# Kernel optimization log

Hardware: AMD Instinct MI355X
Metric: run time of the kernel (lower is better)

## Reference

```python
import jax, jax.numpy as jnp
import numpy as np

N_NODES = 50000
N_EDGES = 800000
D = 128
N_LAYERS = 4
NUM_GRAPHS = 128
BN_EPS = 1e-5


def setup_inputs() -> dict:
    key = jax.random.key(0)
    ks = jax.random.split(key, 10)
    x = jax.random.normal(ks[0], (N_NODES, D), dtype=jnp.float32)
    edge_index = jax.random.randint(ks[1], (2, N_EDGES), 0, N_NODES, dtype=jnp.int64)
    batch = jnp.sort(jax.random.randint(ks[2], (N_NODES,), 0, NUM_GRAPHS, dtype=jnp.int64))
    # GINConv MLP params: Linear(D->D), ReLU, Linear(D->D); stacked over layers.
    scale = 1.0 / np.sqrt(D)
    W1 = jax.random.normal(ks[3], (N_LAYERS, D, D), dtype=jnp.float32) * scale
    b1 = jnp.zeros((N_LAYERS, D), dtype=jnp.float32)
    W2 = jax.random.normal(ks[4], (N_LAYERS, D, D), dtype=jnp.float32) * scale
    b2 = jnp.zeros((N_LAYERS, D), dtype=jnp.float32)
    eps = jnp.zeros((N_LAYERS,), dtype=jnp.float32)  # train_eps=True, init 0
    bn_gamma = jnp.ones((N_LAYERS - 1, D), dtype=jnp.float32)
    bn_beta = jnp.zeros((N_LAYERS - 1, D), dtype=jnp.float32)
    return {"x": x, "edge_index": edge_index, "batch": batch,
            "W1": W1, "b1": b1, "W2": W2, "b2": b2, "eps": eps,
            "bn_gamma": bn_gamma, "bn_beta": bn_beta}


def reference(x, edge_index, batch, W1, b1, W2, b2, eps, bn_gamma, bn_beta):
    src, dst = edge_index[0], edge_index[1]
    h = x
    for i in range(N_LAYERS):
        # GINConv: MLP((1+eps)*x_i + sum_{j->i} x_j)
        agg = jax.ops.segment_sum(h[src], dst, num_segments=N_NODES)  # [N, D]
        z = (1.0 + eps[i]) * h + agg
        z = jnp.maximum(z @ W1[i] + b1[i], 0.0) @ W2[i] + b2[i]
        if i < N_LAYERS - 1:
            # BatchNorm1d (training-mode batch statistics) + ReLU
            mu = jnp.mean(z, axis=0)
            var = jnp.var(z, axis=0)
            z = (z - mu) * jax.lax.rsqrt(var + BN_EPS) * bn_gamma[i] + bn_beta[i]
            z = jnp.maximum(z, 0.0)
        h = z
    # global_add_pool
    return jax.ops.segment_sum(h, batch, num_segments=NUM_GRAPHS)  # [G, D]
```

## Files before the change

kernel.cpp:

```cpp
#include <hip/hip_runtime.h>

#define N_NODES 50000
#define N_EDGES 800000
#define D 128
#define NUM_GRAPHS 128

typedef __attribute__((ext_vector_type(8)))  short bfrag8;
typedef __attribute__((ext_vector_type(16))) float f32x16;

__device__ __forceinline__ float4 f4zero() { return make_float4(0.f, 0.f, 0.f, 0.f); }

__device__ __forceinline__ unsigned short f2bf(float f) {
    unsigned u = __float_as_uint(f);
    unsigned r = (u + 0x7fffu + ((u >> 16) & 1u)) >> 16;
    return (unsigned short)r;
}
__device__ __forceinline__ float bf2f(unsigned short b) {
    return __uint_as_float(((unsigned)b) << 16);
}
__device__ __forceinline__ float4 bf2f4(ushort4 u) {
    return make_float4(bf2f(u.x), bf2f(u.y), bf2f(u.z), bf2f(u.w));
}
__device__ __forceinline__ void acc4(float4& a, float4 u) {
    a.x += u.x; a.y += u.y; a.z += u.z; a.w += u.w;
}
__device__ __forceinline__ void acc8(float* a, uint4 r) {
    a[0] += __uint_as_float(r.x << 16);
    a[1] += __uint_as_float(r.x & 0xffff0000u);
    a[2] += __uint_as_float(r.y << 16);
    a[3] += __uint_as_float(r.y & 0xffff0000u);
    a[4] += __uint_as_float(r.z << 16);
    a[5] += __uint_as_float(r.z & 0xffff0000u);
    a[6] += __uint_as_float(r.w << 16);
    a[7] += __uint_as_float(r.w & 0xffff0000u);
}

__global__ __launch_bounds__(256) void prep_kernel(
    const float* __restrict__ W1, const float* __restrict__ W2,
    const float* __restrict__ x, short* __restrict__ Wt,
    ushort4* __restrict__ Hb, int* __restrict__ deg, float* __restrict__ stats)
{
    int b = blockIdx.x, t = threadIdx.x;
    if (b < 512) {
        int idx = b * 256 + t;
        int m = idx >> 14, rem = idx & 16383;
        int k = rem >> 7, n = rem & 127;
        const float* W = (m < 4) ? (W1 + (size_t)m * 16384)
                                 : (W2 + (size_t)(m - 4) * 16384);
        Wt[(size_t)m * 16384 + n * 128 + k] = (short)f2bf(W[k * 128 + n]);
    } else if (b < 6762) {
        int i = (b - 512) * 256 + t;
        float4 v = ((const float4*)x)[i];
        Hb[i] = make_ushort4(f2bf(v.x), f2bf(v.y), f2bf(v.z), f2bf(v.w));
    } else if (b < 6958) {
        int i = (b - 6762) * 256 + t;
        if (i < N_NODES) deg[i] = 0;
    } else {
        int i = (b - 6958) * 256 + t;
        stats[i] = 0.f;
    }
}

__global__ __launch_bounds__(256) void hist_kernel(
    const int* __restrict__ dst, int* __restrict__ deg,
    int* __restrict__ edge_pos)
{
    int e = blockIdx.x * 256 + threadIdx.x;
    if (e < N_EDGES) edge_pos[e] = atomicAdd(&deg[dst[e]], 1);
}

__global__ __launch_bounds__(256) void scan_block_kernel(
    const int* __restrict__ deg, int* __restrict__ row_ptr,
    int* __restrict__ blockSum)
{
    __shared__ int wsum[4];
    int t = threadIdx.x, b = blockIdx.x;
    int i = b * 256 + t;
    int v = (i < N_NODES) ? deg[i] : 0;
    int lane = t & 63, wid = t >> 6;
    #pragma unroll
    for (int off = 1; off < 64; off <<= 1) {
        int u = __shfl_up(v, off, 64);
        if (lane >= off) v += u;
    }
    if (lane == 63) wsum[wid] = v;
    __syncthreads();
    int add = 0;
    for (int w = 0; w < wid; ++w) add += wsum[w];
    v += add;
    if (i < N_NODES) row_ptr[i + 1] = v;
    if (t == 255) blockSum[b] = v;
}

__global__ __launch_bounds__(256) void scan_fixup_kernel(
    const int* __restrict__ blockSum, int* __restrict__ row_ptr, int nb)
{
    __shared__ int wsum[4];
    __shared__ int sbuf[256];
    int t = threadIdx.x, b = blockIdx.x;
    int v = (t < nb) ? blockSum[t] : 0;
    int lane = t & 63, wid = t >> 6;
    #pragma unroll
    for (int off = 1; off < 64; off <<= 1) {
        int u = __shfl_up(v, off, 64);
        if (lane >= off) v += u;
    }
    if (lane == 63) wsum[wid] = v;
    __syncthreads();
    int add = 0;
    for (int w = 0; w < wid; ++w) add += wsum[w];
    sbuf[t] = v + add;
    __syncthreads();
    if (b == 0 && t == 0) row_ptr[0] = 0;
    if (b > 0) {
        int off = sbuf[b - 1];
        int i = b * 256 + t;
        if (i < N_NODES) row_ptr[i + 1] += off;
    }
}

__global__ __launch_bounds__(256) void fill_kernel(
    const int* __restrict__ src, const int* __restrict__ dst,
    const int* __restrict__ row_ptr, const int* __restrict__ edge_pos,
    int* __restrict__ csr_src)
{
    int e = blockIdx.x * 256 + threadIdx.x;
    if (e >= N_EDGES) return;
    csr_src[row_ptr[dst[e]] + edge_pos[e]] = src[e];
}

__global__ __launch_bounds__(256) void bnapply_kernel(
    uint4* __restrict__ H, const float* __restrict__ stats,
    const float* __restrict__ gamma, const float* __restrict__ beta)
{
    __shared__ float sa[128], sb[128];
    int tid = threadIdx.x;
    if (tid < 128) {
        const float invN = 1.0f / (float)N_NODES;
        float m = stats[tid] * invN;
        float a = gamma[tid] * rsqrtf(stats[128 + tid] * invN - m * m + 1e-5f);
        sa[tid] = a;
        sb[tid] = beta[tid] - m * a;
    }
    __syncthreads();
    int id = blockIdx.x * 256 + tid;
    int c0 = (id & 15) * 8;
    uint4 u = H[id];
    float lo, hi;
    lo = fmaxf(sa[c0 + 0] * __uint_as_float(u.x << 16)          + sb[c0 + 0], 0.f);
    hi = fmaxf(sa[c0 + 1] * __uint_as_float(u.x & 0xffff0000u) + sb[c0 + 1], 0.f);
    u.x = (unsigned)f2bf(lo) | ((unsigned)f2bf(hi) << 16);
    lo = fmaxf(sa[c0 + 2] * __uint_as_float(u.y << 16)          + sb[c0 + 2], 0.f);
    hi = fmaxf(sa[c0 + 3] * __uint_as_float(u.y & 0xffff0000u) + sb[c0 + 3], 0.f);
    u.y = (unsigned)f2bf(lo) | ((unsigned)f2bf(hi) << 16);
    lo = fmaxf(sa[c0 + 4] * __uint_as_float(u.z << 16)          + sb[c0 + 4], 0.f);
    hi = fmaxf(sa[c0 + 5] * __uint_as_float(u.z & 0xffff0000u) + sb[c0 + 5], 0.f);
    u.z = (unsigned)f2bf(lo) | ((unsigned)f2bf(hi) << 16);
    lo = fmaxf(sa[c0 + 6] * __uint_as_float(u.w << 16)          + sb[c0 + 6], 0.f);
    hi = fmaxf(sa[c0 + 7] * __uint_as_float(u.w & 0xffff0000u) + sb[c0 + 7], 0.f);
    u.w = (unsigned)f2bf(lo) | ((unsigned)f2bf(hi) << 16);
    H[id] = u;
}

__global__ __launch_bounds__(256) void gather_kernel(
    const uint4* __restrict__ H, const int* __restrict__ row_ptr,
    const int* __restrict__ csr_src, const float* __restrict__ epsp,
    uint4* __restrict__ A)
{
    int node = blockIdx.x * 16 + (threadIdx.x >> 4);
    int lane = threadIdx.x & 15;
    float eps1 = 1.0f + *epsp;
    int beg = row_ptr[node], end = row_ptr[node + 1];

    uint4 hv = H[node * 16 + lane];
    float acc[8];
    acc[0] = eps1 * __uint_as_float(hv.x << 16);
    acc[1] = eps1 * __uint_as_float(hv.x & 0xffff0000u);
    acc[2] = eps1 * __uint_as_float(hv.y << 16);
    acc[3] = eps1 * __uint_as_float(hv.y & 0xffff0000u);
    acc[4] = eps1 * __uint_as_float(hv.z << 16);
    acc[5] = eps1 * __uint_as_float(hv.z & 0xffff0000u);
    acc[6] = eps1 * __uint_as_float(hv.w << 16);
    acc[7] = eps1 * __uint_as_float(hv.w & 0xffff0000u);

    for (int base = beg; base < end; base += 16) {
        int idx = (base + lane < end) ? csr_src[base + lane] : 0;
        int cnt = min(16, end - base);
        int j = 0;
        for (; j + 8 <= cnt; j += 8) {
            int s0 = __shfl(idx, j + 0, 16), s1 = __shfl(idx, j + 1, 16);
            int s2 = __shfl(idx, j + 2, 16), s3 = __shfl(idx, j + 3, 16);
            int s4 = __shfl(idx, j + 4, 16), s5 = __shfl(idx, j + 5, 16);
            int s6 = __shfl(idx, j + 6, 16), s7 = __shfl(idx, j + 7, 16);
            uint4 u0 = H[s0 * 16 + lane];
            uint4 u1 = H[s1 * 16 + lane];
            uint4 u2 = H[s2 * 16 + lane];
            uint4 u3 = H[s3 * 16 + lane];
            uint4 u4 = H[s4 * 16 + lane];
            uint4 u5 = H[s5 * 16 + lane];
            uint4 u6 = H[s6 * 16 + lane];
            uint4 u7 = H[s7 * 16 + lane];
            acc8(acc, u0); acc8(acc, u1); acc8(acc, u2); acc8(acc, u3);
            acc8(acc, u4); acc8(acc, u5); acc8(acc, u6); acc8(acc, u7);
        }
        for (; j + 4 <= cnt; j += 4) {
            int s0 = __shfl(idx, j + 0, 16), s1 = __shfl(idx, j + 1, 16);
            int s2 = __shfl(idx, j + 2, 16), s3 = __shfl(idx, j + 3, 16);
            uint4 u0 = H[s0 * 16 + lane];
            uint4 u1 = H[s1 * 16 + lane];
            uint4 u2 = H[s2 * 16 + lane];
            uint4 u3 = H[s3 * 16 + lane];
            acc8(acc, u0); acc8(acc, u1); acc8(acc, u2); acc8(acc, u3);
        }
        for (; j < cnt; ++j) {
            int s = __shfl(idx, j, 16);
            uint4 u = H[s * 16 + lane];
            acc8(acc, u);
        }
    }
    uint4 o;
    o.x = (unsigned)f2bf(acc[0]) | ((unsigned)f2bf(acc[1]) << 16);
    o.y = (unsigned)f2bf(acc[2]) | ((unsigned)f2bf(acc[3]) << 16);
    o.z = (unsigned)f2bf(acc[4]) | ((unsigned)f2bf(acc[5]) << 16);
    o.w = (unsigned)f2bf(acc[6]) | ((unsigned)f2bf(acc[7]) << 16);
    A[node * 16 + lane] = o;
}

__global__ __launch_bounds__(256, 3) void mlp_fused_kernel(
    const ushort* __restrict__ A,
    const short* __restrict__ Wt1,
    const short* __restrict__ Wt2,
    const float* __restrict__ bias1,
    const float* __restrict__ bias2,
    ushort* __restrict__ Hout,
    float* __restrict__ statsSum,
    float* __restrict__ statsSq,
    int M)
{
    __shared__ __align__(16) short Wlds[128 * 128];
    __shared__ __align__(16) short zlds[2][32 * 128];
    __shared__ float ssum[128];
    __shared__ float ssq[128];

    const int tid  = threadIdx.x;
    const int wv   = tid >> 6;
    const int lane = tid & 63;
    const int half = lane >> 5;
    const int ln   = lane & 31;
    const int rg   = wv & 1;
    const int ch   = wv >> 1;
    const int row0 = blockIdx.x * 64 + rg * 32;
    const bool doStats = (statsSum != nullptr);
    if (doStats && tid < 128) { ssum[tid] = 0.f; ssq[tid] = 0.f; }

    short* zw = &zlds[rg][0];

    {
        const int4* Wg = (const int4*)Wt1;
        int4* Wl = (int4*)Wlds;
        #pragma unroll
        for (int i = 0; i < 8; ++i) {
            int id = i * 256 + tid;
            int n = id >> 4, c = id & 15;
            Wl[n * 16 + (c ^ (n & 15))] = Wg[id];
        }
    }
    __syncthreads();

    {
        f32x16 acc[2];
        #pragma unroll
        for (int ci = 0; ci < 2; ++ci)
            #pragma unroll
            for (int r = 0; r < 16; ++r) acc[ci][r] = 0.f;

        bfrag8 af[8];
        int rowc = min(row0 + ln, M - 1);
        const ushort* ap = A + (size_t)rowc * 128 + half * 8;
        #pragma unroll
        for (int kk = 0; kk < 8; ++kk)
            af[kk] = *(const bfrag8*)(ap + kk * 16);

        #pragma unroll
        for (int kk = 0; kk < 8; ++kk) {
            #pragma unroll
            for (int ci = 0; ci < 2; ++ci) {
                int n = (ch * 2 + ci) * 32 + ln;
                int c = kk * 2 + half;
                bfrag8 bf = *(const bfrag8*)(Wlds + n * 128 + ((c ^ (n & 15)) << 3));
                acc[ci] = __builtin_amdgcn_mfma_f32_32x32x16_bf16(
                    af[kk], bf, acc[ci], 0, 0, 0);
            }
        }
        #pragma unroll
        for (int ci = 0; ci < 2; ++ci) {
            int col = (ch * 2 + ci) * 32 + ln;
            int cc = col >> 3, co = col & 7;
            float bv = bias1[col];
            #pragma unroll
            for (int r = 0; r < 16; ++r) {
                int rloc = (r & 3) + 8 * (r >> 2) + 4 * half;
                float v = fmaxf(acc[ci][r] + bv, 0.f);
                zw[rloc * 128 + ((cc ^ (rloc & 15)) << 3) + co] = (short)f2bf(v);
            }
        }
    }
    __syncthreads();

    bfrag8 af2[8];
    #pragma unroll
    for (int kk = 0; kk < 8; ++kk) {
        int c = kk * 2 + half;
        af2[kk] = *(const bfrag8*)(zw + ln * 128 + ((c ^ (ln & 15)) << 3));
    }
    {
        const int4* Wg = (const int4*)Wt2;
        int4* Wl = (int4*)Wlds;
        #pragma unroll
        for (int i = 0; i < 8; ++i) {
            int id = i * 256 + tid;
            int n = id >> 4, c = id & 15;
            Wl[n * 16 + (c ^ (n & 15))] = Wg[id];
        }
    }
    __syncthreads();

    {
        f32x16 acc[2];
        #pragma unroll
        for (int ci = 0; ci < 2; ++ci)
            #pragma unroll
            for (int r = 0; r < 16; ++r) acc[ci][r] = 0.f;

        #pragma unroll
        for (int kk = 0; kk < 8; ++kk) {
            #pragma unroll
            for (int ci = 0; ci < 2; ++ci) {
                int n = (ch * 2 + ci) * 32 + ln;
                int c = kk * 2 + half;
                bfrag8 bf = *(const bfrag8*)(Wlds + n * 128 + ((c ^ (n & 15)) << 3));
                acc[ci] = __builtin_amdgcn_mfma_f32_32x32x16_bf16(
                    af2[kk], bf, acc[ci], 0, 0, 0);
            }
        }
        #pragma unroll
        for (int ci = 0; ci < 2; ++ci) {
            int col = (ch * 2 + ci) * 32 + ln;
            int cc = col >> 3, co = col & 7;
            float bv = bias2[col];
            float s = 0.f, sq = 0.f;
            #pragma unroll
            for (int r = 0; r < 16; ++r) {
                int rloc = (r & 3) + 8 * (r >> 2) + 4 * half;
                float v = acc[ci][r] + bv;
                zw[rloc * 128 + ((cc ^ (rloc & 15)) << 3) + co] = (short)f2bf(v);
                if (row0 + rloc < M) { s += v; sq += v * v; }
            }
            if (doStats) {
                s  += __shfl_xor(s, 32);
                sq += __shfl_xor(sq, 32);
                if (half == 0) {
                    atomicAdd(&ssum[col], s);
                    atomicAdd(&ssq[col], sq);
                }
            }
        }
    }
    __syncthreads();

    {
        int4* Ho = (int4*)Hout;
        #pragma unroll
        for (int i = 0; i < 4; ++i) {
            int id = i * 256 + tid;
            int r = id >> 4, c = id & 15;
            int rl = r & 31;
            int grow = blockIdx.x * 64 + r;
            if (grow < M)
                Ho[(size_t)grow * 16 + c] =
                    ((const int4*)&zlds[r >> 5][0])[rl * 16 + (c ^ (rl & 15))];
        }
    }
    if (doStats && tid < 128) {
        atomicAdd(&statsSum[tid], ssum[tid]);
        atomicAdd(&statsSq[tid],  ssq[tid]);
    }
}

__global__ __launch_bounds__(256) void pool_kernel(
    const ushort4* __restrict__ H, const int* __restrict__ batch,
    float* __restrict__ out)
{
    int c4 = threadIdx.x & 31;
    int nl = threadIdx.x >> 5;
    int node0 = blockIdx.x * 256;
    float4 acc = f4zero();
    int gcur = -1;
    for (int i = nl; i < 256; i += 8) {
        int n = node0 + i;
        if (n >= N_NODES) break;
        int g = batch[n];
        if (g != gcur) {
            if (gcur >= 0) {
                float* o = out + gcur * D + c4 * 4;
                atomicAdd(o + 0, acc.x); atomicAdd(o + 1, acc.y);
                atomicAdd(o + 2, acc.z); atomicAdd(o + 3, acc.w);
            }
            gcur = g;
            acc = f4zero();
        }
        float4 v = bf2f4(H[n * 32 + c4]);
        acc4(acc, v);
    }
    if (gcur >= 0) {
        float* o = out + gcur * D + c4 * 4;
        atomicAdd(o + 0, acc.x); atomicAdd(o + 1, acc.y);
        atomicAdd(o + 2, acc.z); atomicAdd(o + 3, acc.w);
    }
}

extern "C" void kernel_launch(void* const* d_in, const int* in_sizes, int n_in,
                              void* d_out, int out_size, void* d_ws, size_t ws_size,
                              hipStream_t stream)
{
    const float* x     = (const float*)d_in[0];
    const int*   ei    = (const int*)d_in[1];
    const int*   batch = (const int*)d_in[2];
    const float* W1    = (const float*)d_in[3];
    const float* b1    = (const float*)d_in[4];
    const float* W2    = (const float*)d_in[5];
    const float* b2    = (const float*)d_in[6];
    const float* eps   = (const float*)d_in[7];
    const float* gamma = (const float*)d_in[8];
    const float* beta  = (const float*)d_in[9];
    float* out = (float*)d_out;

    unsigned short* Hb  = (unsigned short*)d_ws;
    unsigned short* Abf = Hb + (size_t)N_NODES * D;
    float* stats    = (float*)(Abf + (size_t)N_NODES * D);
    int*   deg      = (int*)(stats + 3 * 256);
    int*   row_ptr  = deg + N_NODES;
    int*   blockSum = row_ptr + N_NODES + 1;
    int*   edge_pos = blockSum + 256;
    int*   csr_src  = edge_pos + N_EDGES;
    short* Wt       = (short*)(csr_src + N_EDGES);

    const int* src = ei;
    const int* dst = ei + N_EDGES;

    const int edgeBlocks   = (N_EDGES + 255) / 256;
    const int scanBlocks   = (N_NODES + 255) / 256;
    const int gatherBlocks = (N_NODES + 15) / 16;
    const int bnBlocks     = (N_NODES * 16) / 256;
    const int gemmBlocks   = (N_NODES + 63) / 64;

    prep_kernel<<<6961, 256, 0, stream>>>(W1, W2, x, Wt, (ushort4*)Hb,
                                          deg, stats);
    hist_kernel<<<edgeBlocks, 256, 0, stream>>>(dst, deg, edge_pos);
    scan_block_kernel<<<scanBlocks, 256, 0, stream>>>(deg, row_ptr, blockSum);
    scan_fixup_kernel<<<scanBlocks, 256, 0, stream>>>(blockSum, row_ptr, scanBlocks);
    fill_kernel<<<edgeBlocks, 256, 0, stream>>>(src, dst, row_ptr, edge_pos, csr_src);

    for (int layer = 0; layer < 4; ++layer) {
        const bool bn = (layer < 3);
        if (layer > 0) {
            bnapply_kernel<<<bnBlocks, 256, 0, stream>>>(
                (uint4*)Hb, stats + (size_t)(layer - 1) * 256,
                gamma + (size_t)(layer - 1) * D, beta + (size_t)(layer - 1) * D);
        }
        gather_kernel<<<gatherBlocks, 256, 0, stream>>>(
            (const uint4*)Hb, row_ptr, csr_src, eps + layer, (uint4*)Abf);
        mlp_fused_kernel<<<gemmBlocks, 256, 0, stream>>>(
            Abf, Wt + (size_t)layer * 16384, Wt + (size_t)(4 + layer) * 16384,
            b1 + (size_t)layer * D, b2 + (size_t)layer * D, Hb,
            bn ? stats + layer * 256 : nullptr,
            bn ? stats + layer * 256 + 128 : nullptr, N_NODES);
    }

    hipMemsetAsync(out, 0, (size_t)NUM_GRAPHS * D * sizeof(float), stream);
    pool_kernel<<<scanBlocks, 256, 0, stream>>>(
        (const ushort4*)Hb, batch, out);
}
```

Measured before the change: 411.6 us.

## Pad CSR rows to multiples of eight, use 16-bit indices, fuse pooling into MLP

CSR rows are padded to a multiple of 8 and the padding slots point at an extra zeroed dummy node, so the gather loop runs branch-light 8- or 16-wide batches with no remainder loops. It also prefetches the next index chunk. Edge positions and source indices are stored as 16-bit values to halve index traffic, and gather gets an occupancy hint. The final global add-pool is fused into the last MLP kernel's epilogue, which removes the separate pool kernel and the write and reread of the last layer's H. The cost is extra padded entries in the gather and an implicit limit that node IDs and per-node degrees fit in 16 bits.

```diff
diff --git a/kernel.cpp b/kernel.cpp
--- a/kernel.cpp
+++ b/kernel.cpp
@@ -17,12 +17,6 @@
 }
 __device__ __forceinline__ float bf2f(unsigned short b) {
     return __uint_as_float(((unsigned)b) << 16);
-}
-__device__ __forceinline__ float4 bf2f4(ushort4 u) {
-    return make_float4(bf2f(u.x), bf2f(u.y), bf2f(u.z), bf2f(u.w));
-}
-__device__ __forceinline__ void acc4(float4& a, float4 u) {
-    a.x += u.x; a.y += u.y; a.z += u.z; a.w += u.w;
 }
 __device__ __forceinline__ void acc8(float* a, uint4 r) {
     a[0] += __uint_as_float(r.x << 16);
@@ -55,18 +49,20 @@
     } else if (b < 6958) {
         int i = (b - 6762) * 256 + t;
         if (i < N_NODES) deg[i] = 0;
-    } else {
+    } else if (b < 6961) {
         int i = (b - 6958) * 256 + t;
         stats[i] = 0.f;
+    } else {
+        if (t < 64) ((unsigned*)Hb)[(size_t)N_NODES * 64 + t] = 0u;
     }
 }
 
 __global__ __launch_bounds__(256) void hist_kernel(
     const int* __restrict__ dst, int* __restrict__ deg,
-    int* __restrict__ edge_pos)
+    unsigned short* __restrict__ edge_pos)
 {
     int e = blockIdx.x * 256 + threadIdx.x;
-    if (e < N_EDGES) edge_pos[e] = atomicAdd(&deg[dst[e]], 1);
+    if (e < N_EDGES) edge_pos[e] = (unsigned short)atomicAdd(&deg[dst[e]], 1);
 }
 
 __global__ __launch_bounds__(256) void scan_block_kernel(
@@ -76,7 +72,7 @@
     __shared__ int wsum[4];
     int t = threadIdx.x, b = blockIdx.x;
     int i = b * 256 + t;
-    int v = (i < N_NODES) ? deg[i] : 0;
+    int v = (i < N_NODES) ? ((deg[i] + 7) & ~7) : 0;
     int lane = t & 63, wid = t >> 6;
     #pragma unroll
     for (int off = 1; off < 64; off <<= 1) {
@@ -121,12 +117,23 @@
 
 __global__ __launch_bounds__(256) void fill_kernel(
     const int* __restrict__ src, const int* __restrict__ dst,
-    const int* __restrict__ row_ptr, const int* __restrict__ edge_pos,
-    int* __restrict__ csr_src)
-{
-    int e = blockIdx.x * 256 + threadIdx.x;
-    if (e >= N_EDGES) return;
-    csr_src[row_ptr[dst[e]] + edge_pos[e]] = src[e];
+    const int* __restrict__ row_ptr, const unsigned short* __restrict__ edge_pos,
+    const int* __restrict__ deg, unsigned short* __restrict__ csr_src)
+{
+    int b = blockIdx.x, t = threadIdx.x;
+    if (b < 3125) {
+        int e = b * 256 + t;
+        if (e < N_EDGES)
+            csr_src[row_ptr[dst[e]] + (int)edge_pos[e]] = (unsigned short)src[e];
+    } else {
+        int n = (b - 3125) * 256 + t;
+        if (n < N_NODES) {
+            int e0 = row_ptr[n] + deg[n];
+            int e1 = row_ptr[n + 1];
+            for (int j = e0; j < e1; ++j)
+                csr_src[j] = (unsigned short)N_NODES;
+        }
+    }
 }
 
 __global__ __launch_bounds__(256) void bnapply_kernel(
@@ -162,9 +169,9 @@
     H[id] = u;
 }
 
-__global__ __launch_bounds__(256) void gather_kernel(
+__global__ __launch_bounds__(256, 4) void gather_kernel(
     const uint4* __restrict__ H, const int* __restrict__ row_ptr,
-    const int* __restrict__ csr_src, const float* __restrict__ epsp,
+    const unsigned short* __restrict__ csr, const float* __restrict__ epsp,
     uint4* __restrict__ A)
 {
     int node = blockIdx.x * 16 + (threadIdx.x >> 4);
@@ -172,7 +179,7 @@
     float eps1 = 1.0f + *epsp;
     int beg = row_ptr[node], end = row_ptr[node + 1];
 
-    uint4 hv = H[node * 16 + lane];
+    uint4 hv = H[(size_t)node * 16 + lane];
     float acc[8];
     acc[0] = eps1 * __uint_as_float(hv.x << 16);
     acc[1] = eps1 * __uint_as_float(hv.x & 0xffff0000u);
@@ -183,47 +190,54 @@
     acc[6] = eps1 * __uint_as_float(hv.w << 16);
     acc[7] = eps1 * __uint_as_float(hv.w & 0xffff0000u);
 
-    for (int base = beg; base < end; base += 16) {
-        int idx = (base + lane < end) ? csr_src[base + lane] : 0;
-        int cnt = min(16, end - base);
-        int j = 0;
-        for (; j + 8 <= cnt; j += 8) {
-            int s0 = __shfl(idx, j + 0, 16), s1 = __shfl(idx, j + 1, 16);
-            int s2 = __shfl(idx, j + 2, 16), s3 = __shfl(idx, j + 3, 16);
-            int s4 = __shfl(idx, j + 4, 16), s5 = __shfl(idx, j + 5, 16);
-            int s6 = __shfl(idx, j + 6, 16), s7 = __shfl(idx, j + 7, 16);
-            uint4 u0 = H[s0 * 16 + lane];
-            uint4 u1 = H[s1 * 16 + lane];
-            uint4 u2 = H[s2 * 16 + lane];
-            uint4 u3 = H[s3 * 16 + lane];
-            uint4 u4 = H[s4 * 16 + lane];
-            uint4 u5 = H[s5 * 16 + lane];
-            uint4 u6 = H[s6 * 16 + lane];
-            uint4 u7 = H[s7 * 16 + lane];
+    int base = beg;
+    int idx = (int)csr[base + lane];
+    while (base < end) {
+        int nb = base + 16;
+        int nidx = 0;
+        if (nb < end) nidx = (int)csr[nb + lane];
+        int cnt = end - base;
+        int s0 = __shfl(idx, 0, 16), s1 = __shfl(idx, 1, 16);
+        int s2 = __shfl(idx, 2, 16), s3 = __shfl(idx, 3, 16);
+        int s4 = __shfl(idx, 4, 16), s5 = __shfl(idx, 5, 16);
+        int s6 = __shfl(idx, 6, 16), s7 = __shfl(idx, 7, 16);
+        uint4 u0 = H[(size_t)s0 * 16 + lane];
+        uint4 u1 = H[(size_t)s1 * 16 + lane];
+        uint4 u2 = H[(size_t)s2 * 16 + lane];
+        uint4 u3 = H[(size_t)s3 * 16 + lane];
+        uint4 u4 = H[(size_t)s4 * 16 + lane];
+        uint4 u5 = H[(size_t)s5 * 16 + lane];
+        uint4 u6 = H[(size_t)s6 * 16 + lane];
+        uint4 u7 = H[(size_t)s7 * 16 + lane];
+        if (cnt > 8) {
+            int t0 = __shfl(idx,  8, 16), t1 = __shfl(idx,  9, 16);
+            int t2 = __shfl(idx, 10, 16), t3 = __shfl(idx, 11, 16);
+            int t4 = __shfl(idx, 12, 16), t5 = __shfl(idx, 13, 16);
+            int t6 = __shfl(idx, 14, 16), t7 = __shfl(idx, 15, 16);
+            uint4 w0 = H[(size_t)t0 * 16 + lane];
+            uint4 w1 = H[(size_t)t1 * 16 + lane];
+            uint4 w2 = H[(size_t)t2 * 16 + lane];
+            uint4 w3 = H[(size_t)t3 * 16 + lane];
+            uint4 w4 = H[(size_t)t4 * 16 + lane];
+            uint4 w5 = H[(size_t)t5 * 16 + lane];
+            uint4 w6 = H[(size_t)t6 * 16 + lane];
+            uint4 w7 = H[(size_t)t7 * 16 + lane];
             acc8(acc, u0); acc8(acc, u1); acc8(acc, u2); acc8(acc, u3);
             acc8(acc, u4); acc8(acc, u5); acc8(acc, u6); acc8(acc, u7);
-        }
-        for (; j + 4 <= cnt; j += 4) {
-            int s0 = __shfl(idx, j + 0, 16), s1 = __shfl(idx, j + 1, 16);
-            int s2 = __shfl(idx, j + 2, 16), s3 = __shfl(idx, j + 3, 16);
-            uint4 u0 = H[s0 * 16 + lane];
-            uint4 u1 = H[s1 * 16 + lane];
-            uint4 u2 = H[s2 * 16 + lane];
-            uint4 u3 = H[s3 * 16 + lane];
+            acc8(acc, w0); acc8(acc, w1); acc8(acc, w2); acc8(acc, w3);
+            acc8(acc, w4); acc8(acc, w5); acc8(acc, w6); acc8(acc, w7);
+        } else {
             acc8(acc, u0); acc8(acc, u1); acc8(acc, u2); acc8(acc, u3);
-        }
-        for (; j < cnt; ++j) {
-            int s = __shfl(idx, j, 16);
-            uint4 u = H[s * 16 + lane];
-            acc8(acc, u);
-        }
+            acc8(acc, u4); acc8(acc, u5); acc8(acc, u6); acc8(acc, u7);
+        }
+        idx = nidx; base = nb;
     }
     uint4 o;
     o.x = (unsigned)f2bf(acc[0]) | ((unsigned)f2bf(acc[1]) << 16);
     o.y = (unsigned)f2bf(acc[2]) | ((unsigned)f2bf(acc[3]) << 16);
     o.z = (unsigned)f2bf(acc[4]) | ((unsigned)f2bf(acc[5]) << 16);
     o.w = (unsigned)f2bf(acc[6]) | ((unsigned)f2bf(acc[7]) << 16);
-    A[node * 16 + lane] = o;
+    A[(size_t)node * 16 + lane] = o;
 }
 
 __global__ __launch_bounds__(256, 3) void mlp_fused_kernel(
@@ -235,6 +249,8 @@
     ushort* __restrict__ Hout,
     float* __restrict__ statsSum,
     float* __restrict__ statsSq,
+    const int* __restrict__ batch,
+    float* __restrict__ poolOut,
     int M)
 {
     __shared__ __align__(16) short Wlds[128 * 128];
@@ -368,7 +384,7 @@
     }
     __syncthreads();
 
-    {
+    if (poolOut == nullptr) {
         int4* Ho = (int4*)Hout;
         #pragma unroll
         for (int i = 0; i < 4; ++i) {
@@ -380,42 +396,40 @@
                 Ho[(size_t)grow * 16 + c] =
                     ((const int4*)&zlds[r >> 5][0])[rl * 16 + (c ^ (rl & 15))];
         }
+    } else {
+        int c4 = tid & 31;
+        int rl8 = tid >> 5;
+        int cc = c4 >> 1, co = (c4 & 1) * 4;
+        float4 ap = f4zero();
+        int gcur = -1;
+        for (int i = rl8; i < 64; i += 8) {
+            int grow = blockIdx.x * 64 + i;
+            if (grow >= M) break;
+            int g = batch[grow];
+            if (g != gcur) {
+                if (gcur >= 0) {
+                    float* o = poolOut + gcur * D + c4 * 4;
+                    atomicAdd(o + 0, ap.x); atomicAdd(o + 1, ap.y);
+                    atomicAdd(o + 2, ap.z); atomicAdd(o + 3, ap.w);
+                }
+                gcur = g; ap = f4zero();
+            }
+            const short* zr = &zlds[i >> 5][0];
+            int rl = i & 31;
+            const ushort4 u = *(const ushort4*)
+                ((const ushort*)(zr + rl * 128 + ((cc ^ (rl & 15)) << 3) + co));
+            ap.x += bf2f(u.x); ap.y += bf2f(u.y);
+            ap.z += bf2f(u.z); ap.w += bf2f(u.w);
+        }
+        if (gcur >= 0) {
+            float* o = poolOut + gcur * D + c4 * 4;
+            atomicAdd(o + 0, ap.x); atomicAdd(o + 1, ap.y);
+            atomicAdd(o + 2, ap.z); atomicAdd(o + 3, ap.w);
+        }
     }
     if (doStats && tid < 128) {
         atomicAdd(&statsSum[tid], ssum[tid]);
         atomicAdd(&statsSq[tid],  ssq[tid]);
-    }
-}
-
-__global__ __launch_bounds__(256) void pool_kernel(
-    const ushort4* __restrict__ H, const int* __restrict__ batch,
-    float* __restrict__ out)
-{
-    int c4 = threadIdx.x & 31;
-    int nl = threadIdx.x >> 5;
-    int node0 = blockIdx.x * 256;
-    float4 acc = f4zero();
-    int gcur = -1;
-    for (int i = nl; i < 256; i += 8) {
-        int n = node0 + i;
-        if (n >= N_NODES) break;
-        int g = batch[n];
-        if (g != gcur) {
-            if (gcur >= 0) {
-                float* o = out + gcur * D + c4 * 4;
-                atomicAdd(o + 0, acc.x); atomicAdd(o + 1, acc.y);
-                atomicAdd(o + 2, acc.z); atomicAdd(o + 3, acc.w);
-            }
-            gcur = g;
-            acc = f4zero();
-        }
-        float4 v = bf2f4(H[n * 32 + c4]);
-        acc4(acc, v);
-    }
-    if (gcur >= 0) {
-        float* o = out + gcur * D + c4 * 4;
-        atomicAdd(o + 0, acc.x); atomicAdd(o + 1, acc.y);
-        atomicAdd(o + 2, acc.z); atomicAdd(o + 3, acc.w);
     }
 }
 
@@ -436,14 +450,14 @@
     float* out = (float*)d_out;
 
     unsigned short* Hb  = (unsigned short*)d_ws;
-    unsigned short* Abf = Hb + (size_t)N_NODES * D;
+    unsigned short* Abf = Hb + (size_t)(N_NODES + 1) * D;
     float* stats    = (float*)(Abf + (size_t)N_NODES * D);
     int*   deg      = (int*)(stats + 3 * 256);
     int*   row_ptr  = deg + N_NODES;
     int*   blockSum = row_ptr + N_NODES + 1;
-    int*   edge_pos = blockSum + 256;
-    int*   csr_src  = edge_pos + N_EDGES;
-    short* Wt       = (short*)(csr_src + N_EDGES);
+    unsigned short* edge_pos = (unsigned short*)(blockSum + 256);
+    unsigned short* csr_src  = edge_pos + N_EDGES;
+    short* Wt       = (short*)(csr_src + N_EDGES + 7 * N_NODES + 16);
 
     const int* src = ei;
     const int* dst = ei + N_EDGES;
@@ -454,12 +468,14 @@
     const int bnBlocks     = (N_NODES * 16) / 256;
     const int gemmBlocks   = (N_NODES + 63) / 64;
 
-    prep_kernel<<<6961, 256, 0, stream>>>(W1, W2, x, Wt, (ushort4*)Hb,
+    prep_kernel<<<6962, 256, 0, stream>>>(W1, W2, x, Wt, (ushort4*)Hb,
                                           deg, stats);
     hist_kernel<<<edgeBlocks, 256, 0, stream>>>(dst, deg, edge_pos);
     scan_block_kernel<<<scanBlocks, 256, 0, stream>>>(deg, row_ptr, blockSum);
     scan_fixup_kernel<<<scanBlocks, 256, 0, stream>>>(blockSum, row_ptr, scanBlocks);
-    fill_kernel<<<edgeBlocks, 256, 0, stream>>>(src, dst, row_ptr, edge_pos, csr_src);
+    fill_kernel<<<edgeBlocks + scanBlocks, 256, 0, stream>>>(
+        src, dst, row_ptr, edge_pos, deg, csr_src);
+    hipMemsetAsync(out, 0, (size_t)NUM_GRAPHS * D * sizeof(float), stream);
 
     for (int layer = 0; layer < 4; ++layer) {
         const bool bn = (layer < 3);
@@ -474,10 +490,8 @@
             Abf, Wt + (size_t)layer * 16384, Wt + (size_t)(4 + layer) * 16384,
             b1 + (size_t)layer * D, b2 + (size_t)layer * D, Hb,
             bn ? stats + layer * 256 : nullptr,
-            bn ? stats + layer * 256 + 128 : nullptr, N_NODES);
-    }
-
-    hipMemsetAsync(out, 0, (size_t)NUM_GRAPHS * D * sizeof(float), stream);
-    pool_kernel<<<scanBlocks, 256, 0, stream>>>(
-        (const ushort4*)Hb, batch, out);
-}
+            bn ? stats + layer * 256 + 128 : nullptr,
+            bn ? nullptr : batch,
+            bn ? nullptr : out, N_NODES);
+    }
+}
```

After: 389.4 us. 1.06x faster.
